# Optimization experiments

Measured on AMD Instinct MI355X. Metric: run time of the kernel, lower is better.

## Reference

```python
import jax, jax.numpy as jnp
import numpy as np

B, N, D = 32, 1024, 512

def setup_inputs() -> dict:
    key = jax.random.key(0)
    ks = jax.random.split(key, 5)
    s = 1.0 / np.sqrt(D)
    return {
        "x": jax.random.normal(ks[0], (B, N, D), jnp.float32),
        "Wq": jax.random.normal(ks[1], (D, D), jnp.float32) * s,
        "bq": jnp.zeros((D,), jnp.float32),
        "Wk": jax.random.normal(ks[2], (D, D), jnp.float32) * s,
        "bk": jnp.zeros((D,), jnp.float32),
        "Wv": jax.random.normal(ks[3], (D, D), jnp.float32) * s,
        "bv": jnp.zeros((D,), jnp.float32),
        "pos_bias": jax.random.normal(ks[4], (N, N), jnp.float32) * 0.02,
    }

def reference(x, Wq, bq, Wk, bk, Wv, bv, pos_bias):
    # torch nn.Linear: y = x @ W.T + b
    q = x @ Wq.T + bq                      # [B,N,D]
    k = x @ Wk.T + bk                      # [B,N,D]
    v = x @ Wv.T + bv                      # [B,N,D]
    # AFT-full: out[b,t,d] = sig(q)[b,t,d] * sum_s exp(k[b,s,d]+w[t,s]) v[b,s,d]
    #                                        / sum_s exp(k[b,s,d]+w[t,s])
    # exp(k+w) factors as exp(w)*exp(k); the num/den ratio is invariant to
    # per-row shifts of w and per-(b,d) shifts of k, so stabilize both.
    w = pos_bias - jnp.max(pos_bias, axis=1, keepdims=True)   # [T,S]
    kk = k - jnp.max(k, axis=1, keepdims=True)                # [B,S,D]
    ew = jnp.exp(w)
    ek = jnp.exp(kk)
    num = jnp.einsum('ts,bsd->btd', ew, ek * v)               # [B,T,D]
    den = jnp.einsum('ts,bsd->btd', ew, ek)                   # [B,T,D]
    return jax.nn.sigmoid(q) * (num / den)
```

## Files before the change

### kernel.cpp

```cpp
#include <hip/hip_runtime.h>

typedef unsigned short u16;
typedef unsigned int u32;
using frag8 = __attribute__((ext_vector_type(8))) short;
using f32x4 = __attribute__((ext_vector_type(4))) float;

__device__ __forceinline__ u16 f2bf(float f) {
  union { float f; u32 u; } x;
  x.f = f;
  u32 r = (x.u + 0x7fffu + ((x.u >> 16) & 1u)) >> 16;
  return (u16)r;
}

__device__ __forceinline__ void stage_tile64(const u16* g, int ld, u16* lds, int tid) {
  const int wv = tid >> 6;
#pragma unroll
  for (int i = 0; i < 4; ++i) {
    const int c = i * 256 + tid;
    const int row = c >> 3;
    const int colc = (c & 7) ^ (row & 7);
    __builtin_amdgcn_global_load_lds(
        (const __attribute__((address_space(1))) void*)(g + (size_t)row * ld + colc * 8),
        (__attribute__((address_space(3))) void*)(lds + (size_t)(i * 256 + wv * 64) * 8),
        16, 0, 0);
  }
}

__device__ __forceinline__ frag8 frag_read64(const u16* lds, int row, int kk, int quad) {
  const int cc = (kk * 4 + quad) ^ (row & 7);
  return *(const frag8*)&lds[row * 64 + cc * 8];
}

__global__ void prep_kernel(const float* __restrict__ x, const float* __restrict__ Wq,
                            const float* __restrict__ Wk, const float* __restrict__ Wv,
                            const float* __restrict__ pb, u16* __restrict__ xb,
                            u16* __restrict__ wqb, u16* __restrict__ wkb,
                            u16* __restrict__ wvb, u16* __restrict__ ewb) {
  const int blk = blockIdx.x;
  const float* src;
  u16* dst;
  int base;
  bool ex = false;
  if (blk < 16384)      { src = x;  dst = xb;  base = blk; }
  else if (blk < 16640) { src = Wq; dst = wqb; base = blk - 16384; }
  else if (blk < 16896) { src = Wk; dst = wkb; base = blk - 16640; }
  else if (blk < 17152) { src = Wv; dst = wvb; base = blk - 16896; }
  else                  { src = pb; dst = ewb; base = blk - 17152; ex = true; }
  const int i = base * 256 + threadIdx.x;
  float4 v = ((const float4*)src)[i];
  ushort4 o;
  if (ex) {
    o.x = f2bf(__expf(v.x)); o.y = f2bf(__expf(v.y));
    o.z = f2bf(__expf(v.z)); o.w = f2bf(__expf(v.w));
  } else {
    o.x = f2bf(v.x); o.y = f2bf(v.y); o.z = f2bf(v.z); o.w = f2bf(v.w);
  }
  ((ushort4*)dst)[i] = o;
}

__global__ __launch_bounds__(256, 3) void q_kernel(const u16* __restrict__ xb,
                                                   const u16* __restrict__ wqb,
                                                   const float* __restrict__ bq,
                                                   float* __restrict__ out) {
  __shared__ __align__(16) u16 As[128 * 64];
  __shared__ __align__(16) u16 Bs[128 * 64];
  const int tid = threadIdx.x;
  const int lane = tid & 63, wv = tid >> 6;
  const int wm = (wv & 1) * 64, wn = (wv >> 1) * 64;
  const int fr = lane & 15, quad = lane >> 4;
  const int m0 = blockIdx.y * 128;
  const int n0 = blockIdx.x * 128;
  f32x4 acc[4][4] = {};
  for (int k0 = 0; k0 < 512; k0 += 64) {
    stage_tile64(xb + (size_t)m0 * 512 + k0, 512, As, tid);
    stage_tile64(wqb + (size_t)n0 * 512 + k0, 512, Bs, tid);
    __syncthreads();
#pragma unroll
    for (int kk = 0; kk < 2; ++kk) {
      frag8 a[4], b[4];
#pragma unroll
      for (int i = 0; i < 4; ++i) {
        a[i] = frag_read64(As, wm + i * 16 + fr, kk, quad);
        b[i] = frag_read64(Bs, wn + i * 16 + fr, kk, quad);
      }
#pragma unroll
      for (int mi = 0; mi < 4; ++mi)
#pragma unroll
        for (int ni = 0; ni < 4; ++ni)
          acc[mi][ni] = __builtin_amdgcn_mfma_f32_16x16x32_bf16(a[mi], b[ni], acc[mi][ni], 0, 0, 0);
    }
    __syncthreads();
  }
#pragma unroll
  for (int mi = 0; mi < 4; ++mi)
#pragma unroll
    for (int ni = 0; ni < 4; ++ni) {
      const int col = n0 + wn + ni * 16 + fr;
      const float bqv = bq[col];
#pragma unroll
      for (int r = 0; r < 4; ++r) {
        const int row = m0 + wm + mi * 16 + quad * 4 + r;
        const float qv = acc[mi][ni][r] + bqv;
        out[(size_t)row * 512 + col] = 1.0f / (1.0f + __expf(-qv));
      }
    }
}

__global__ __launch_bounds__(256, 2) void kv_kernel(const u16* __restrict__ xb,
                                                    const u16* __restrict__ wkb,
                                                    const u16* __restrict__ wvb,
                                                    const float* __restrict__ bk,
                                                    const float* __restrict__ bv,
                                                    u16* __restrict__ ekT,
                                                    u16* __restrict__ ekvT) {
  __shared__ __align__(16) u16 Ak[128 * 64];
  __shared__ __align__(16) u16 Av[128 * 64];
  __shared__ __align__(16) u16 Bs[128 * 64];
  const int tid = threadIdx.x;
  const int lane = tid & 63, wv = tid >> 6;
  const int wm = (wv & 1) * 64, wn = (wv >> 1) * 64;
  const int fr = lane & 15, quad = lane >> 4;
  const int s0 = blockIdx.x * 128;
  const int d0 = blockIdx.y * 128;
  const int b  = blockIdx.z;
  f32x4 acck[4][4] = {}, accv[4][4] = {};
  for (int k0 = 0; k0 < 512; k0 += 64) {
    stage_tile64(wkb + (size_t)d0 * 512 + k0, 512, Ak, tid);
    stage_tile64(wvb + (size_t)d0 * 512 + k0, 512, Av, tid);
    stage_tile64(xb + ((size_t)b * 1024 + s0) * 512 + k0, 512, Bs, tid);
    __syncthreads();
#pragma unroll
    for (int kk = 0; kk < 2; ++kk) {
      frag8 ak[4], av[4], bb[4];
#pragma unroll
      for (int i = 0; i < 4; ++i) {
        ak[i] = frag_read64(Ak, wm + i * 16 + fr, kk, quad);
        av[i] = frag_read64(Av, wm + i * 16 + fr, kk, quad);
        bb[i] = frag_read64(Bs, wn + i * 16 + fr, kk, quad);
      }
#pragma unroll
      for (int mi = 0; mi < 4; ++mi)
#pragma unroll
        for (int ni = 0; ni < 4; ++ni) {
          acck[mi][ni] = __builtin_amdgcn_mfma_f32_16x16x32_bf16(ak[mi], bb[ni], acck[mi][ni], 0, 0, 0);
          accv[mi][ni] = __builtin_amdgcn_mfma_f32_16x16x32_bf16(av[mi], bb[ni], accv[mi][ni], 0, 0, 0);
        }
    }
    __syncthreads();
  }
#pragma unroll
  for (int mi = 0; mi < 4; ++mi)
#pragma unroll
    for (int r = 0; r < 4; ++r) {
      const int d = d0 + wm + mi * 16 + quad * 4 + r;
      const float bkv = bk[d], bvv = bv[d];
#pragma unroll
      for (int ni = 0; ni < 4; ++ni) {
        const int s = s0 + wn + ni * 16 + fr;
        const float ek = __expf(acck[mi][ni][r] + bkv);
        const float vv = accv[mi][ni][r] + bvv;
        const size_t idx = ((size_t)b * 512 + d) * 1024 + s;
        ekT[idx]  = f2bf(ek);
        ekvT[idx] = f2bf(ek * vv);
      }
    }
}

__global__ __launch_bounds__(256, 2) void aft_kernel(const u16* __restrict__ ew,
                                                     const u16* __restrict__ ekT,
                                                     const u16* __restrict__ ekvT,
                                                     float* __restrict__ out) {
  __shared__ __align__(16) u16 As[128 * 64];
  __shared__ __align__(16) u16 B1[128 * 64];
  __shared__ __align__(16) u16 B2[128 * 64];
  const int tid = threadIdx.x;
  const int lane = tid & 63, wv = tid >> 6;
  const int wm = (wv & 1) * 64, wn = (wv >> 1) * 64;
  const int fr = lane & 15, quad = lane >> 4;
  const int d0 = blockIdx.x * 128;
  const int t0 = blockIdx.y * 128;
  const int b  = blockIdx.z;
  f32x4 accn[4][4] = {}, accd[4][4] = {};
  for (int k0 = 0; k0 < 1024; k0 += 64) {
    stage_tile64(ew + (size_t)t0 * 1024 + k0, 1024, As, tid);
    stage_tile64(ekvT + ((size_t)b * 512 + d0) * 1024 + k0, 1024, B1, tid);
    stage_tile64(ekT + ((size_t)b * 512 + d0) * 1024 + k0, 1024, B2, tid);
    __syncthreads();
#pragma unroll
    for (int kk = 0; kk < 2; ++kk) {
      frag8 a[4], b1[4], b2[4];
#pragma unroll
      for (int i = 0; i < 4; ++i) {
        a[i]  = frag_read64(As, wm + i * 16 + fr, kk, quad);
        b1[i] = frag_read64(B1, wn + i * 16 + fr, kk, quad);
        b2[i] = frag_read64(B2, wn + i * 16 + fr, kk, quad);
      }
#pragma unroll
      for (int mi = 0; mi < 4; ++mi)
#pragma unroll
        for (int ni = 0; ni < 4; ++ni) {
          accn[mi][ni] = __builtin_amdgcn_mfma_f32_16x16x32_bf16(a[mi], b1[ni], accn[mi][ni], 0, 0, 0);
          accd[mi][ni] = __builtin_amdgcn_mfma_f32_16x16x32_bf16(a[mi], b2[ni], accd[mi][ni], 0, 0, 0);
        }
    }
    __syncthreads();
  }
#pragma unroll
  for (int mi = 0; mi < 4; ++mi)
#pragma unroll
    for (int ni = 0; ni < 4; ++ni)
#pragma unroll
      for (int r = 0; r < 4; ++r) {
        const int t = t0 + wm + mi * 16 + quad * 4 + r;
        const int d = d0 + wn + ni * 16 + fr;
        const size_t idx = ((size_t)b * 1024 + t) * 512 + d;
        const float sq = out[idx];
        out[idx] = sq * accn[mi][ni][r] / accd[mi][ni][r];
      }
}

extern "C" void kernel_launch(void* const* d_in, const int* in_sizes, int n_in,
                              void* d_out, int out_size, void* d_ws, size_t ws_size,
                              hipStream_t stream) {
  const float* x  = (const float*)d_in[0];
  const float* Wq = (const float*)d_in[1];
  const float* bq = (const float*)d_in[2];
  const float* Wk = (const float*)d_in[3];
  const float* bk = (const float*)d_in[4];
  const float* Wv = (const float*)d_in[5];
  const float* bv = (const float*)d_in[6];
  const float* pb = (const float*)d_in[7];
  float* out = (float*)d_out;
  char* ws = (char*)d_ws;
  u16* xb   = (u16*)(ws);
  u16* wqb  = (u16*)(ws + 33554432);
  u16* wkb  = (u16*)(ws + 34078720);
  u16* wvb  = (u16*)(ws + 34603008);
  u16* ewb  = (u16*)(ws + 35127296);
  u16* ekT  = (u16*)(ws + 37224448);
  u16* ekvT = (u16*)(ws + 70778880);

  prep_kernel<<<18176, 256, 0, stream>>>(x, Wq, Wk, Wv, pb, xb, wqb, wkb, wvb, ewb);
  q_kernel<<<dim3(4, 256), 256, 0, stream>>>(xb, wqb, bq, out);
  kv_kernel<<<dim3(8, 4, 32), 256, 0, stream>>>(xb, wkb, wvb, bk, bv, ekT, ekvT);
  aft_kernel<<<dim3(4, 8, 32), 256, 0, stream>>>(ewb, ekT, ekvT, out);
}
```

Before: 253.6 us.

## Fuse Q projection and sigmoid into the AFT kernel, drop separate q_kernel

```diff
diff --git a/kernel.cpp b/kernel.cpp
--- a/kernel.cpp
+++ b/kernel.cpp
@@ -58,54 +58,6 @@
   ((ushort4*)dst)[i] = o;
 }
 
-__global__ __launch_bounds__(256, 3) void q_kernel(const u16* __restrict__ xb,
-                                                   const u16* __restrict__ wqb,
-                                                   const float* __restrict__ bq,
-                                                   float* __restrict__ out) {
-  __shared__ __align__(16) u16 As[128 * 64];
-  __shared__ __align__(16) u16 Bs[128 * 64];
-  const int tid = threadIdx.x;
-  const int lane = tid & 63, wv = tid >> 6;
-  const int wm = (wv & 1) * 64, wn = (wv >> 1) * 64;
-  const int fr = lane & 15, quad = lane >> 4;
-  const int m0 = blockIdx.y * 128;
-  const int n0 = blockIdx.x * 128;
-  f32x4 acc[4][4] = {};
-  for (int k0 = 0; k0 < 512; k0 += 64) {
-    stage_tile64(xb + (size_t)m0 * 512 + k0, 512, As, tid);
-    stage_tile64(wqb + (size_t)n0 * 512 + k0, 512, Bs, tid);
-    __syncthreads();
-#pragma unroll
-    for (int kk = 0; kk < 2; ++kk) {
-      frag8 a[4], b[4];
-#pragma unroll
-      for (int i = 0; i < 4; ++i) {
-        a[i] = frag_read64(As, wm + i * 16 + fr, kk, quad);
-        b[i] = frag_read64(Bs, wn + i * 16 + fr, kk, quad);
-      }
-#pragma unroll
-      for (int mi = 0; mi < 4; ++mi)
-#pragma unroll
-        for (int ni = 0; ni < 4; ++ni)
-          acc[mi][ni] = __builtin_amdgcn_mfma_f32_16x16x32_bf16(a[mi], b[ni], acc[mi][ni], 0, 0, 0);
-    }
-    __syncthreads();
-  }
-#pragma unroll
-  for (int mi = 0; mi < 4; ++mi)
-#pragma unroll
-    for (int ni = 0; ni < 4; ++ni) {
-      const int col = n0 + wn + ni * 16 + fr;
-      const float bqv = bq[col];
-#pragma unroll
-      for (int r = 0; r < 4; ++r) {
-        const int row = m0 + wm + mi * 16 + quad * 4 + r;
-        const float qv = acc[mi][ni][r] + bqv;
-        out[(size_t)row * 512 + col] = 1.0f / (1.0f + __expf(-qv));
-      }
-    }
-}
-
 __global__ __launch_bounds__(256, 2) void kv_kernel(const u16* __restrict__ xb,
                                                     const u16* __restrict__ wkb,
                                                     const u16* __restrict__ wvb,
@@ -169,31 +121,71 @@
 __global__ __launch_bounds__(256, 2) void aft_kernel(const u16* __restrict__ ew,
                                                      const u16* __restrict__ ekT,
                                                      const u16* __restrict__ ekvT,
+                                                     const u16* __restrict__ xb,
+                                                     const u16* __restrict__ wqb,
+                                                     const float* __restrict__ bq,
                                                      float* __restrict__ out) {
-  __shared__ __align__(16) u16 As[128 * 64];
-  __shared__ __align__(16) u16 B1[128 * 64];
-  __shared__ __align__(16) u16 B2[128 * 64];
+  __shared__ __align__(16) u16 T0[128 * 64];
+  __shared__ __align__(16) u16 T1[128 * 64];
+  __shared__ __align__(16) u16 T2[128 * 64];
   const int tid = threadIdx.x;
   const int lane = tid & 63, wv = tid >> 6;
   const int wm = (wv & 1) * 64, wn = (wv >> 1) * 64;
   const int fr = lane & 15, quad = lane >> 4;
-  const int d0 = blockIdx.x * 128;
+  const int n0 = blockIdx.x * 128;
   const int t0 = blockIdx.y * 128;
   const int b  = blockIdx.z;
+
+  f32x4 qacc[4][4] = {};
+  const u16* xrow = xb + ((size_t)b * 1024 + t0) * 512;
+  for (int k0 = 0; k0 < 512; k0 += 64) {
+    stage_tile64(xrow + k0, 512, T0, tid);
+    stage_tile64(wqb + (size_t)n0 * 512 + k0, 512, T1, tid);
+    __syncthreads();
+#pragma unroll
+    for (int kk = 0; kk < 2; ++kk) {
+      frag8 a[4], w[4];
+#pragma unroll
+      for (int i = 0; i < 4; ++i) {
+        a[i] = frag_read64(T0, wm + i * 16 + fr, kk, quad);
+        w[i] = frag_read64(T1, wn + i * 16 + fr, kk, quad);
+      }
+#pragma unroll
+      for (int mi = 0; mi < 4; ++mi)
+#pragma unroll
+        for (int ni = 0; ni < 4; ++ni)
+          qacc[mi][ni] = __builtin_amdgcn_mfma_f32_16x16x32_bf16(a[mi], w[ni], qacc[mi][ni], 0, 0, 0);
+    }
+    __syncthreads();
+  }
+  u32 pk[4][4][2];
+#pragma unroll
+  for (int mi = 0; mi < 4; ++mi)
+#pragma unroll
+    for (int ni = 0; ni < 4; ++ni) {
+      const float bqv = bq[n0 + wn + ni * 16 + fr];
+#pragma unroll
+      for (int h = 0; h < 2; ++h) {
+        const float s0v = 1.0f / (1.0f + __expf(-(qacc[mi][ni][2 * h] + bqv)));
+        const float s1v = 1.0f / (1.0f + __expf(-(qacc[mi][ni][2 * h + 1] + bqv)));
+        pk[mi][ni][h] = (u32)f2bf(s0v) | ((u32)f2bf(s1v) << 16);
+      }
+    }
+
   f32x4 accn[4][4] = {}, accd[4][4] = {};
   for (int k0 = 0; k0 < 1024; k0 += 64) {
-    stage_tile64(ew + (size_t)t0 * 1024 + k0, 1024, As, tid);
-    stage_tile64(ekvT + ((size_t)b * 512 + d0) * 1024 + k0, 1024, B1, tid);
-    stage_tile64(ekT + ((size_t)b * 512 + d0) * 1024 + k0, 1024, B2, tid);
+    stage_tile64(ew + (size_t)t0 * 1024 + k0, 1024, T0, tid);
+    stage_tile64(ekvT + ((size_t)b * 512 + n0) * 1024 + k0, 1024, T1, tid);
+    stage_tile64(ekT + ((size_t)b * 512 + n0) * 1024 + k0, 1024, T2, tid);
     __syncthreads();
 #pragma unroll
     for (int kk = 0; kk < 2; ++kk) {
       frag8 a[4], b1[4], b2[4];
 #pragma unroll
       for (int i = 0; i < 4; ++i) {
-        a[i]  = frag_read64(As, wm + i * 16 + fr, kk, quad);
-        b1[i] = frag_read64(B1, wn + i * 16 + fr, kk, quad);
-        b2[i] = frag_read64(B2, wn + i * 16 + fr, kk, quad);
+        a[i]  = frag_read64(T0, wm + i * 16 + fr, kk, quad);
+        b1[i] = frag_read64(T1, wn + i * 16 + fr, kk, quad);
+        b2[i] = frag_read64(T2, wn + i * 16 + fr, kk, quad);
       }
 #pragma unroll
       for (int mi = 0; mi < 4; ++mi)
@@ -212,10 +204,12 @@
 #pragma unroll
       for (int r = 0; r < 4; ++r) {
         const int t = t0 + wm + mi * 16 + quad * 4 + r;
-        const int d = d0 + wn + ni * 16 + fr;
-        const size_t idx = ((size_t)b * 1024 + t) * 512 + d;
-        const float sq = out[idx];
-        out[idx] = sq * accn[mi][ni][r] / accd[mi][ni][r];
+        const int d = n0 + wn + ni * 16 + fr;
+        const u32 p = pk[mi][ni][r >> 1];
+        const u32 bits = (r & 1) ? (p & 0xffff0000u) : (p << 16);
+        union { u32 u; float f; } sq;
+        sq.u = bits;
+        out[((size_t)b * 1024 + t) * 512 + d] = sq.f * accn[mi][ni][r] / accd[mi][ni][r];
       }
 }
 
@@ -241,7 +235,6 @@
   u16* ekvT = (u16*)(ws + 70778880);
 
   prep_kernel<<<18176, 256, 0, stream>>>(x, Wq, Wk, Wv, pb, xb, wqb, wkb, wvb, ewb);
-  q_kernel<<<dim3(4, 256), 256, 0, stream>>>(xb, wqb, bq, out);
   kv_kernel<<<dim3(8, 4, 32), 256, 0, stream>>>(xb, wkb, wvb, bk, bv, ekT, ekvT);
-  aft_kernel<<<dim3(4, 8, 32), 256, 0, stream>>>(ewb, ekT, ekvT, out);
-}
+  aft_kernel<<<dim3(4, 8, 32), 256, 0, stream>>>(ewb, ekT, ekvT, xb, wqb, bq, out);
+}
```

Result: slower. 271.1 us (+6.9%).
